# Kernel tuning notes

Measured on AMD Instinct MI355X. Metric: run time of the kernel, lower is better.

## Reference

```python
import jax, jax.numpy as jnp
import numpy as np

EPS = 1e-6
B, T, E, H = 2, 512, 1024, 256
NUM_BLOCK = 12


def normalize(x):
    # RMS-style normalization over the feature dim (no learned affine)
    return x * jax.lax.rsqrt(jnp.mean(x * x, axis=-1, keepdims=True) + EPS)


def bar_quadratic_causal(a, b):
    # y_i = (1/i) * sum_{j<=i} relu(a_i + b_j)   (causal prefix mean of pairwise relation)
    # a, b: [B, T, H]
    Tn = a.shape[1]
    pair = jax.nn.relu(a[:, :, None, :] + b[:, None, :, :])  # [B, T(i), T(j), H]
    mask = jnp.tril(jnp.ones((Tn, Tn), dtype=a.dtype))        # causal j<=i
    s = jnp.einsum('bijh,ij->bih', pair, mask)
    counts = jnp.arange(1, Tn + 1, dtype=a.dtype)[None, :, None]
    return s / counts


def setup_inputs() -> dict:
    key = jax.random.key(0)
    k0, k1, k2, k3 = jax.random.split(key, 4)
    x = jax.random.normal(k0, (B, T, E), dtype=jnp.float32)
    w1 = jax.random.normal(k1, (E, H), dtype=jnp.float32) * 0.02
    b1 = jnp.zeros((H,), dtype=jnp.float32)
    w2 = jax.random.normal(k2, (E, H), dtype=jnp.float32) * 0.02
    b2 = jnp.zeros((H,), dtype=jnp.float32)
    w3 = jax.random.normal(k3, (H, E), dtype=jnp.float32) * (0.02 / np.sqrt(NUM_BLOCK))
    b3 = jnp.zeros((E,), dtype=jnp.float32)
    return {"x": x, "w1": w1, "b1": b1, "w2": w2, "b2": b2, "w3": w3, "b3": b3}


def reference(x, w1, b1, w2, b2, w3, b3):
    r = normalize(x)
    a = r @ w1 + b1
    b = r @ w2 + b2
    # PreNorm == 'approx': normalize a and b separately
    a = normalize(a)
    b = normalize(b)
    r = bar_quadratic_causal(a, b)
    # PostNorm == 'yes'
    r = normalize(r)
    r = r @ w3 + b3
    return x + r
```

## Files before the change

kernel.cpp:

```cpp
#include <hip/hip_runtime.h>

#define EPSF 1e-6f
#define Bsz 2
#define Tn  512
#define En  1024
#define Hn  256
#define Mtot (Bsz * Tn)
typedef unsigned short us_t;
typedef unsigned int   u32_t;

typedef __attribute__((ext_vector_type(8))) short bf16x8;
typedef __attribute__((ext_vector_type(4))) float f32x4;
#define MFMA16(a, b, c) __builtin_amdgcn_mfma_f32_16x16x32_bf16((a), (b), (c), 0, 0, 0)

__device__ __forceinline__ us_t f2bf(float f) {
  union { float f; u32_t u; } x; x.f = f;
  u32_t r = (x.u + 0x7fffu + ((x.u >> 16) & 1u)) >> 16;
  return (us_t)r;
}
__device__ __forceinline__ float bf2f(us_t u) {
  union { u32_t u; float f; } x; x.u = ((u32_t)u) << 16; return x.f;
}
__device__ __forceinline__ uint2 pack4bf(float a, float b, float c, float d) {
  uint2 r;
  r.x = (u32_t)f2bf(a) | ((u32_t)f2bf(b) << 16);
  r.y = (u32_t)f2bf(c) | ((u32_t)f2bf(d) << 16);
  return r;
}
__device__ __forceinline__ float block_reduce_sum_256(float v, float* smem) {
  #pragma unroll
  for (int off = 32; off > 0; off >>= 1) v += __shfl_down(v, off, 64);
  const int wave = threadIdx.x >> 6;
  if ((threadIdx.x & 63) == 0) smem[wave] = v;
  __syncthreads();
  float s = smem[0] + smem[1] + smem[2] + smem[3];
  __syncthreads();
  return s;
}

__global__ __launch_bounds__(256) void k_prep(
    const float* __restrict__ x,
    const float* __restrict__ w1, const float* __restrict__ w2,
    const float* __restrict__ w3,
    us_t* __restrict__ xb, float* __restrict__ rs,
    us_t* __restrict__ w1t, us_t* __restrict__ w2t, us_t* __restrict__ w3t)
{
  const int b = blockIdx.x, t = threadIdx.x;

  if (b < 256) {
    const int wid = t >> 6, lane = t & 63;
    const int row = b * 4 + wid;
    const float4* xp = (const float4*)(x + (size_t)row * En);
    float4 v[4];
    #pragma unroll
    for (int i = 0; i < 4; ++i) v[i] = xp[lane + 64 * i];
    float ss = 0.f;
    #pragma unroll
    for (int i = 0; i < 4; ++i)
      ss += v[i].x*v[i].x + v[i].y*v[i].y + v[i].z*v[i].z + v[i].w*v[i].w;
    #pragma unroll
    for (int off = 32; off > 0; off >>= 1) ss += __shfl_xor(ss, off, 64);
    if (lane == 0) rs[row] = rsqrtf(ss * (1.0f / En) + EPSF);
    uint2* xo = (uint2*)(xb + (size_t)row * En);
    #pragma unroll
    for (int i = 0; i < 4; ++i)
      xo[lane + 64 * i] = pack4bf(v[i].x, v[i].y, v[i].z, v[i].w);
    return;
  }

  __shared__ float ts[32][33];
  const int i = b - 256;
  const float* src; us_t* dst; int R, C, tr, tc;
  if (i < 256)      { src = w1; dst = w1t; R = 1024; C = 256;  tr = i >> 3;  tc = i & 7; }
  else if (i < 512) { int k = i - 256; src = w2; dst = w2t; R = 1024; C = 256; tr = k >> 3; tc = k & 7; }
  else              { int k = i - 512; src = w3; dst = w3t; R = 256; C = 1024; tr = k >> 5; tc = k & 31; }

  const int r = t >> 3, c4 = (t & 7) * 4;
  float4 v = *(const float4*)(src + (size_t)(tr * 32 + r) * C + tc * 32 + c4);
  ts[r][c4 + 0] = v.x; ts[r][c4 + 1] = v.y; ts[r][c4 + 2] = v.z; ts[r][c4 + 3] = v.w;
  __syncthreads();
  float o0 = ts[c4 + 0][r], o1 = ts[c4 + 1][r], o2 = ts[c4 + 2][r], o3 = ts[c4 + 3][r];
  *(uint2*)(dst + (size_t)(tc * 32 + r) * R + tr * 32 + c4) = pack4bf(o0, o1, o2, o3);
}

__global__ __launch_bounds__(256, 4) void k_gemm(
    const us_t* __restrict__ xb,
    const us_t* __restrict__ w1t, const us_t* __restrict__ w2t,
    float* __restrict__ Praw)
{
  const int blk = blockIdx.x;
  const int mt = blk >> 4, nt = blk & 15;
  const int m0 = mt * 16, n0 = nt * 32;
  const int wid = threadIdx.x >> 6, lane = threadIdx.x & 63;
  const int lg = lane >> 4, lr = lane & 15;
  const int k0 = wid * 256;

  const us_t* ap = xb + (size_t)(m0 + lr) * En + k0 + lg * 8;
  const us_t* bbase = (n0 < Hn) ? (w1t + (size_t)n0 * En)
                                : (w2t + (size_t)(n0 - Hn) * En);
  const us_t* bp0 = bbase + (size_t)lr * En + k0 + lg * 8;
  const us_t* bp1 = bp0 + (size_t)16 * En;

  f32x4 acc0 = {0.f,0.f,0.f,0.f}, acc1 = acc0;

  #pragma unroll
  for (int s = 0; s < 8; ++s) {
    bf16x8 a  = *(const bf16x8*)(ap  + s * 32);
    bf16x8 b0 = *(const bf16x8*)(bp0 + s * 32);
    bf16x8 b1 = *(const bf16x8*)(bp1 + s * 32);
    acc0 = MFMA16(a, b0, acc0);
    acc1 = MFMA16(a, b1, acc1);
  }

  __shared__ float cmb[4][16][32];
  #pragma unroll
  for (int i = 0; i < 4; ++i) {
    cmb[wid][lg * 4 + i][lr]      = acc0[i];
    cmb[wid][lg * 4 + i][16 + lr] = acc1[i];
  }
  __syncthreads();

  #pragma unroll
  for (int e = 0; e < 2; ++e) {
    const int idx = threadIdx.x + e * 256;
    const int row = idx >> 5, col = idx & 31;
    float s = cmb[0][row][col] + cmb[1][row][col]
            + cmb[2][row][col] + cmb[3][row][col];
    Praw[(size_t)(m0 + row) * 512 + n0 + col] = s;
  }
}

__global__ __launch_bounds__(256) void k_norm(
    const float* __restrict__ Praw, const float* __restrict__ rs,
    const float* __restrict__ b1, const float* __restrict__ b2,
    us_t* __restrict__ A, us_t* __restrict__ BmT)
{
  const int rw = blockIdx.x * 4 + (threadIdx.x >> 6);
  const int lane = threadIdx.x & 63;
  const int which = rw >> 10, r = rw & 1023;
  const int h0 = lane * 4;

  float4 d = *(const float4*)(Praw + (size_t)r * 512 + which * Hn + h0);
  const float s0 = rs[r];
  const float* bias = which ? b2 : b1;
  float4 bv = *(const float4*)(bias + h0);
  float vx = d.x * s0 + bv.x, vy = d.y * s0 + bv.y;
  float vz = d.z * s0 + bv.z, vw = d.w * s0 + bv.w;

  float ss = vx*vx + vy*vy + vz*vz + vw*vw;
  #pragma unroll
  for (int o2 = 32; o2 > 0; o2 >>= 1) ss += __shfl_xor(ss, o2, 64);
  const float sc = rsqrtf(ss * (1.0f / Hn) + EPSF);

  if (!which) {
    *(uint2*)(A + (size_t)r * Hn + h0) = pack4bf(vx*sc, vy*sc, vz*sc, vw*sc);
  } else {
    const int bb = r >> 9, tcol = r & 511;
    us_t* bt = BmT + (size_t)bb * Hn * Tn + tcol;
    bt[(size_t)(h0 + 0) * Tn] = f2bf(vx * sc);
    bt[(size_t)(h0 + 1) * Tn] = f2bf(vy * sc);
    bt[(size_t)(h0 + 2) * Tn] = f2bf(vz * sc);
    bt[(size_t)(h0 + 3) * Tn] = f2bf(vw * sc);
  }
}

#define JCHB 32
__global__ __launch_bounds__(256) void k_bar(
    const us_t* __restrict__ A, const us_t* __restrict__ BmT,
    us_t* __restrict__ Yb)
{
  const int raw = blockIdx.x;
  const int sel = (raw < 256) ? raw : (511 - raw);
  const int bb  = raw >> 8;
  const int i0  = sel * 2;
  const int h   = threadIdx.x;
  const size_t baseA = (size_t)bb * Tn * Hn;
  const us_t* __restrict__ bt = BmT + (size_t)bb * Hn * Tn + (size_t)h * Tn;

  float av0 = bf2f(A[baseA + (size_t)i0 * Hn + h]);
  float av1 = bf2f(A[baseA + (size_t)(i0 + 1) * Hn + h]);
  float sum0 = 0.f, sum1 = 0.f;

  const int nfull = i0 & ~(JCHB - 1);
  bf16x8 c0[4], c1[4];

  #define LOADC(dst, jj) { _Pragma("unroll") \
    for (int q = 0; q < 4; ++q) dst[q] = *(const bf16x8*)(bt + (jj) + q * 8); }
  #define PROCF(srcb) { _Pragma("unroll") \
    for (int q = 0; q < 4; ++q) { _Pragma("unroll") \
      for (int e = 0; e < 8; ++e) { \
        float bv = bf2f((us_t)srcb[q][e]); \
        sum0 += fmaxf(av0 + bv, 0.f); \
        sum1 += fmaxf(av1 + bv, 0.f); } } }

  if (nfull > 0) {
    LOADC(c0, 0);
    int j = 0;
    while (true) {
      const bool m1 = (j + JCHB     < nfull);
      const bool m2 = (j + 2 * JCHB < nfull);
      if (m1) LOADC(c1, j + JCHB);
      PROCF(c0);
      j += JCHB;
      if (!m1) break;
      if (m2) LOADC(c0, j + JCHB);
      PROCF(c1);
      j += JCHB;
      if (!m2) break;
    }
  }
  {
    bf16x8 ct[4];
    LOADC(ct, nfull);
    const int lim = i0 - nfull;
    #pragma unroll
    for (int q = 0; q < 4; ++q)
      #pragma unroll
      for (int e = 0; e < 8; ++e) {
        const int jl = q * 8 + e;
        float bv = bf2f((us_t)ct[q][e]);
        sum0 += (jl <= lim)     ? fmaxf(av0 + bv, 0.f) : 0.f;
        sum1 += (jl <= lim + 1) ? fmaxf(av1 + bv, 0.f) : 0.f;
      }
  }
  #undef LOADC
  #undef PROCF

  __shared__ float red[4];
  {
    float ss = block_reduce_sum_256(sum0 * sum0, red);
    float c  = (float)(i0 + 1);
    float sc = rsqrtf(ss * (1.0f / Hn) + EPSF * c * c);
    Yb[baseA + (size_t)i0 * Hn + h] = f2bf(sum0 * sc);
  }
  {
    float ss = block_reduce_sum_256(sum1 * sum1, red);
    float c  = (float)(i0 + 2);
    float sc = rsqrtf(ss * (1.0f / Hn) + EPSF * c * c);
    Yb[baseA + (size_t)(i0 + 1) * Hn + h] = f2bf(sum1 * sc);
  }
}

__global__ __launch_bounds__(256, 4) void k_out(
    const us_t* __restrict__ Yb, const us_t* __restrict__ w3t,
    const float* __restrict__ x, const float* __restrict__ b3,
    float* __restrict__ out)
{
  const int wid = threadIdx.x >> 6, lane = threadIdx.x & 63;
  const int wg = blockIdx.x * 4 + wid;
  const int nt = wg & 31, mt = wg >> 5;
  const int m0 = mt * 16, n0 = nt * 32;
  const int lg = lane >> 4, lr = lane & 15;

  const us_t* ap  = Yb  + (size_t)(m0 + lr) * Hn + lg * 8;
  const us_t* bp0 = w3t + (size_t)(n0 + lr) * Hn + lg * 8;
  const us_t* bp1 = bp0 + (size_t)16 * Hn;

  f32x4 acc0 = {0.f,0.f,0.f,0.f}, acc1 = acc0;

  #pragma unroll
  for (int s = 0; s < 8; ++s) {
    bf16x8 a  = *(const bf16x8*)(ap  + s * 32);
    bf16x8 b0 = *(const bf16x8*)(bp0 + s * 32);
    bf16x8 b1 = *(const bf16x8*)(bp1 + s * 32);
    acc0 = MFMA16(a, b0, acc0);
    acc1 = MFMA16(a, b1, acc1);
  }

  const int row = m0 + lg * 4;
  const int c0 = n0 + lr, c1 = n0 + 16 + lr;
  const float bv0 = b3[c0], bv1 = b3[c1];
  #pragma unroll
  for (int i = 0; i < 4; ++i) {
    const size_t o0 = (size_t)(row + i) * En + c0;
    const size_t o1 = (size_t)(row + i) * En + c1;
    out[o0] = x[o0] + acc0[i] + bv0;
    out[o1] = x[o1] + acc1[i] + bv1;
  }
}

extern "C" void kernel_launch(void* const* d_in, const int* in_sizes, int n_in,
                              void* d_out, int out_size, void* d_ws, size_t ws_size,
                              hipStream_t stream) {
  const float* x  = (const float*)d_in[0];
  const float* w1 = (const float*)d_in[1];
  const float* b1 = (const float*)d_in[2];
  const float* w2 = (const float*)d_in[3];
  const float* b2 = (const float*)d_in[4];
  const float* w3 = (const float*)d_in[5];
  const float* b3 = (const float*)d_in[6];
  float* out = (float*)d_out;

  char* q = (char*)d_ws;
  float* Praw = (float*)q;  q += (size_t)Mtot * 512 * 4;
  us_t* xb    = (us_t*)q;   q += (size_t)Mtot * En * 2;
  us_t* w1t   = (us_t*)q;   q += (size_t)Hn * En * 2;
  us_t* w2t   = (us_t*)q;   q += (size_t)Hn * En * 2;
  us_t* w3t   = (us_t*)q;   q += (size_t)En * Hn * 2;
  us_t* A     = (us_t*)q;   q += (size_t)Mtot * Hn * 2;
  us_t* BmT   = (us_t*)q;   q += (size_t)Mtot * Hn * 2;
  us_t* Yb    = (us_t*)q;   q += (size_t)Mtot * Hn * 2;
  float* rs   = (float*)q;  q += (size_t)Mtot * 4;

  k_prep<<<1024, 256, 0, stream>>>(x, w1, w2, w3, xb, rs, w1t, w2t, w3t);
  k_gemm<<<1024, 256, 0, stream>>>(xb, w1t, w2t, Praw);
  k_norm<<<512,  256, 0, stream>>>(Praw, rs, b1, b2, A, BmT);
  k_bar <<<512,  256, 0, stream>>>(A, BmT, Yb);
  k_out <<<512,  256, 0, stream>>>(Yb, w3t, x, b3, out);
}
```

Before: 47.64 us.

## Switch to fp16 storage with packed-half bar loop, coalesced BmT transpose, finer k_out tiles

Stores intermediates in fp16 instead of bf16 and uses fp16 MFMA. The quadratic bar loop now does relu-add in packed half2 arithmetic, accumulating four pairs in fp16 before widening to fp32, which roughly halves the ALU work of the dominant kernel. k_norm writes the transposed B matrix through shared memory with 8-byte stores instead of strided 2-byte scatters. k_out uses 16x16 tiles per wave and twice as many blocks for more parallelism. The partial fp16 accumulation and the fp16 range of x could cost accuracy.

```diff
diff --git a/kernel.cpp b/kernel.cpp
--- a/kernel.cpp
+++ b/kernel.cpp
@@ -9,22 +9,23 @@
 typedef unsigned short us_t;
 typedef unsigned int   u32_t;
 
-typedef __attribute__((ext_vector_type(8))) short bf16x8;
-typedef __attribute__((ext_vector_type(4))) float f32x4;
-#define MFMA16(a, b, c) __builtin_amdgcn_mfma_f32_16x16x32_bf16((a), (b), (c), 0, 0, 0)
-
-__device__ __forceinline__ us_t f2bf(float f) {
-  union { float f; u32_t u; } x; x.f = f;
-  u32_t r = (x.u + 0x7fffu + ((x.u >> 16) & 1u)) >> 16;
-  return (us_t)r;
-}
-__device__ __forceinline__ float bf2f(us_t u) {
-  union { u32_t u; float f; } x; x.u = ((u32_t)u) << 16; return x.f;
-}
-__device__ __forceinline__ uint2 pack4bf(float a, float b, float c, float d) {
+typedef __attribute__((ext_vector_type(8))) __fp16 f16x8;
+typedef __attribute__((ext_vector_type(2))) __fp16 h2_t;
+typedef __attribute__((ext_vector_type(8))) short  short8;
+typedef __attribute__((ext_vector_type(4))) float  f32x4;
+#define MFMA16(a, b, c) __builtin_amdgcn_mfma_f32_16x16x32_f16((a), (b), (c), 0, 0, 0)
+
+__device__ __forceinline__ us_t f2h(float f) {
+  __fp16 h = (__fp16)f;
+  return __builtin_bit_cast(us_t, h);
+}
+__device__ __forceinline__ float h2f(us_t u) {
+  return (float)__builtin_bit_cast(__fp16, u);
+}
+__device__ __forceinline__ uint2 pack4h(float a, float b, float c, float d) {
   uint2 r;
-  r.x = (u32_t)f2bf(a) | ((u32_t)f2bf(b) << 16);
-  r.y = (u32_t)f2bf(c) | ((u32_t)f2bf(d) << 16);
+  r.x = (u32_t)f2h(a) | ((u32_t)f2h(b) << 16);
+  r.y = (u32_t)f2h(c) | ((u32_t)f2h(d) << 16);
   return r;
 }
 __device__ __forceinline__ float block_reduce_sum_256(float v, float* smem) {
@@ -64,7 +65,7 @@
     uint2* xo = (uint2*)(xb + (size_t)row * En);
     #pragma unroll
     for (int i = 0; i < 4; ++i)
-      xo[lane + 64 * i] = pack4bf(v[i].x, v[i].y, v[i].z, v[i].w);
+      xo[lane + 64 * i] = pack4h(v[i].x, v[i].y, v[i].z, v[i].w);
     return;
   }
 
@@ -80,7 +81,7 @@
   ts[r][c4 + 0] = v.x; ts[r][c4 + 1] = v.y; ts[r][c4 + 2] = v.z; ts[r][c4 + 3] = v.w;
   __syncthreads();
   float o0 = ts[c4 + 0][r], o1 = ts[c4 + 1][r], o2 = ts[c4 + 2][r], o3 = ts[c4 + 3][r];
-  *(uint2*)(dst + (size_t)(tc * 32 + r) * R + tr * 32 + c4) = pack4bf(o0, o1, o2, o3);
+  *(uint2*)(dst + (size_t)(tc * 32 + r) * R + tr * 32 + c4) = pack4h(o0, o1, o2, o3);
 }
 
 __global__ __launch_bounds__(256, 4) void k_gemm(
@@ -105,9 +106,9 @@
 
   #pragma unroll
   for (int s = 0; s < 8; ++s) {
-    bf16x8 a  = *(const bf16x8*)(ap  + s * 32);
-    bf16x8 b0 = *(const bf16x8*)(bp0 + s * 32);
-    bf16x8 b1 = *(const bf16x8*)(bp1 + s * 32);
+    f16x8 a  = *(const f16x8*)(ap  + s * 32);
+    f16x8 b0 = *(const f16x8*)(bp0 + s * 32);
+    f16x8 b1 = *(const f16x8*)(bp1 + s * 32);
     acc0 = MFMA16(a, b0, acc0);
     acc1 = MFMA16(a, b1, acc1);
   }
@@ -135,15 +136,33 @@
     const float* __restrict__ b1, const float* __restrict__ b2,
     us_t* __restrict__ A, us_t* __restrict__ BmT)
 {
-  const int rw = blockIdx.x * 4 + (threadIdx.x >> 6);
-  const int lane = threadIdx.x & 63;
-  const int which = rw >> 10, r = rw & 1023;
+  const int blk = blockIdx.x, t = threadIdx.x;
+  const int wid = t >> 6, lane = t & 63;
   const int h0 = lane * 4;
 
-  float4 d = *(const float4*)(Praw + (size_t)r * 512 + which * Hn + h0);
+  if (blk < 256) {
+    const int r = blk * 4 + wid;
+    float4 d = *(const float4*)(Praw + (size_t)r * 512 + h0);
+    const float s0 = rs[r];
+    float4 bv = *(const float4*)(b1 + h0);
+    float vx = d.x * s0 + bv.x, vy = d.y * s0 + bv.y;
+    float vz = d.z * s0 + bv.z, vw = d.w * s0 + bv.w;
+
+    float ss = vx*vx + vy*vy + vz*vz + vw*vw;
+    #pragma unroll
+    for (int o2 = 32; o2 > 0; o2 >>= 1) ss += __shfl_xor(ss, o2, 64);
+    const float sc = rsqrtf(ss * (1.0f / Hn) + EPSF);
+    *(uint2*)(A + (size_t)r * Hn + h0) = pack4h(vx*sc, vy*sc, vz*sc, vw*sc);
+    return;
+  }
+
+  __shared__ us_t ls[4][256];
+  const int r0 = (blk - 256) * 4;
+  const int r  = r0 + wid;
+
+  float4 d = *(const float4*)(Praw + (size_t)r * 512 + Hn + h0);
   const float s0 = rs[r];
-  const float* bias = which ? b2 : b1;
-  float4 bv = *(const float4*)(bias + h0);
+  float4 bv = *(const float4*)(b2 + h0);
   float vx = d.x * s0 + bv.x, vy = d.y * s0 + bv.y;
   float vz = d.z * s0 + bv.z, vw = d.w * s0 + bv.w;
 
@@ -152,16 +171,15 @@
   for (int o2 = 32; o2 > 0; o2 >>= 1) ss += __shfl_xor(ss, o2, 64);
   const float sc = rsqrtf(ss * (1.0f / Hn) + EPSF);
 
-  if (!which) {
-    *(uint2*)(A + (size_t)r * Hn + h0) = pack4bf(vx*sc, vy*sc, vz*sc, vw*sc);
-  } else {
-    const int bb = r >> 9, tcol = r & 511;
-    us_t* bt = BmT + (size_t)bb * Hn * Tn + tcol;
-    bt[(size_t)(h0 + 0) * Tn] = f2bf(vx * sc);
-    bt[(size_t)(h0 + 1) * Tn] = f2bf(vy * sc);
-    bt[(size_t)(h0 + 2) * Tn] = f2bf(vz * sc);
-    bt[(size_t)(h0 + 3) * Tn] = f2bf(vw * sc);
-  }
+  *(uint2*)&ls[wid][h0] = pack4h(vx*sc, vy*sc, vz*sc, vw*sc);
+  __syncthreads();
+
+  const int h = t;
+  u32_t w0  = (u32_t)ls[0][h] | ((u32_t)ls[1][h] << 16);
+  u32_t w1v = (u32_t)ls[2][h] | ((u32_t)ls[3][h] << 16);
+  const int bb   = r0 >> 9;
+  const int tcol = r0 & 511;
+  *(uint2*)(BmT + (size_t)bb * Hn * Tn + (size_t)h * Tn + tcol) = make_uint2(w0, w1v);
 }
 
 #define JCHB 32
@@ -177,21 +195,32 @@
   const size_t baseA = (size_t)bb * Tn * Hn;
   const us_t* __restrict__ bt = BmT + (size_t)bb * Hn * Tn + (size_t)h * Tn;
 
-  float av0 = bf2f(A[baseA + (size_t)i0 * Hn + h]);
-  float av1 = bf2f(A[baseA + (size_t)(i0 + 1) * Hn + h]);
+  const __fp16 a0h = __builtin_bit_cast(__fp16, A[baseA + (size_t)i0 * Hn + h]);
+  const __fp16 a1h = __builtin_bit_cast(__fp16, A[baseA + (size_t)(i0 + 1) * Hn + h]);
+  const float av0 = (float)a0h;
+  const float av1 = (float)a1h;
+  h2_t z2;  z2[0]  = (__fp16)0.f; z2[1]  = (__fp16)0.f;
+  h2_t a02; a02[0] = a0h;         a02[1] = a0h;
+  h2_t a12; a12[0] = a1h;         a12[1] = a1h;
   float sum0 = 0.f, sum1 = 0.f;
 
   const int nfull = i0 & ~(JCHB - 1);
-  bf16x8 c0[4], c1[4];
+  short8 c0[4], c1[4];
 
   #define LOADC(dst, jj) { _Pragma("unroll") \
-    for (int q = 0; q < 4; ++q) dst[q] = *(const bf16x8*)(bt + (jj) + q * 8); }
-  #define PROCF(srcb) { _Pragma("unroll") \
-    for (int q = 0; q < 4; ++q) { _Pragma("unroll") \
-      for (int e = 0; e < 8; ++e) { \
-        float bv = bf2f((us_t)srcb[q][e]); \
-        sum0 += fmaxf(av0 + bv, 0.f); \
-        sum1 += fmaxf(av1 + bv, 0.f); } } }
+    for (int q = 0; q < 4; ++q) dst[q] = *(const short8*)(bt + (jj) + q * 8); }
+  #define PROCP(buf) { _Pragma("unroll") \
+    for (int q = 0; q < 4; ++q) { \
+      const h2_t* ph = (const h2_t*)&buf[q]; \
+      h2_t p0 = z2, p1 = z2; \
+      _Pragma("unroll") \
+      for (int w2i = 0; w2i < 4; ++w2i) { \
+        h2_t bv2 = ph[w2i]; \
+        p0 += __builtin_elementwise_max(a02 + bv2, z2); \
+        p1 += __builtin_elementwise_max(a12 + bv2, z2); \
+      } \
+      sum0 += (float)p0[0] + (float)p0[1]; \
+      sum1 += (float)p1[0] + (float)p1[1]; } }
 
   if (nfull > 0) {
     LOADC(c0, 0);
@@ -200,17 +229,17 @@
       const bool m1 = (j + JCHB     < nfull);
       const bool m2 = (j + 2 * JCHB < nfull);
       if (m1) LOADC(c1, j + JCHB);
-      PROCF(c0);
+      PROCP(c0);
       j += JCHB;
       if (!m1) break;
       if (m2) LOADC(c0, j + JCHB);
-      PROCF(c1);
+      PROCP(c1);
       j += JCHB;
       if (!m2) break;
     }
   }
   {
-    bf16x8 ct[4];
+    short8 ct[4];
     LOADC(ct, nfull);
     const int lim = i0 - nfull;
     #pragma unroll
@@ -218,26 +247,26 @@
       #pragma unroll
       for (int e = 0; e < 8; ++e) {
         const int jl = q * 8 + e;
-        float bv = bf2f((us_t)ct[q][e]);
+        float bv = h2f((us_t)ct[q][e]);
         sum0 += (jl <= lim)     ? fmaxf(av0 + bv, 0.f) : 0.f;
         sum1 += (jl <= lim + 1) ? fmaxf(av1 + bv, 0.f) : 0.f;
       }
   }
   #undef LOADC
-  #undef PROCF
+  #undef PROCP
 
   __shared__ float red[4];
   {
     float ss = block_reduce_sum_256(sum0 * sum0, red);
     float c  = (float)(i0 + 1);
     float sc = rsqrtf(ss * (1.0f / Hn) + EPSF * c * c);
-    Yb[baseA + (size_t)i0 * Hn + h] = f2bf(sum0 * sc);
+    Yb[baseA + (size_t)i0 * Hn + h] = f2h(sum0 * sc);
   }
   {
     float ss = block_reduce_sum_256(sum1 * sum1, red);
     float c  = (float)(i0 + 2);
     float sc = rsqrtf(ss * (1.0f / Hn) + EPSF * c * c);
-    Yb[baseA + (size_t)(i0 + 1) * Hn + h] = f2bf(sum1 * sc);
+    Yb[baseA + (size_t)(i0 + 1) * Hn + h] = f2h(sum1 * sc);
   }
 }
 
@@ -248,34 +277,29 @@
 {
   const int wid = threadIdx.x >> 6, lane = threadIdx.x & 63;
   const int wg = blockIdx.x * 4 + wid;
-  const int nt = wg & 31, mt = wg >> 5;
-  const int m0 = mt * 16, n0 = nt * 32;
+  const int nt = wg & 63, mt = wg >> 6;
+  const int m0 = mt * 16, n0 = nt * 16;
   const int lg = lane >> 4, lr = lane & 15;
 
-  const us_t* ap  = Yb  + (size_t)(m0 + lr) * Hn + lg * 8;
-  const us_t* bp0 = w3t + (size_t)(n0 + lr) * Hn + lg * 8;
-  const us_t* bp1 = bp0 + (size_t)16 * Hn;
-
-  f32x4 acc0 = {0.f,0.f,0.f,0.f}, acc1 = acc0;
+  const us_t* ap = Yb  + (size_t)(m0 + lr) * Hn + lg * 8;
+  const us_t* bp = w3t + (size_t)(n0 + lr) * Hn + lg * 8;
+
+  f32x4 acc = {0.f,0.f,0.f,0.f};
 
   #pragma unroll
   for (int s = 0; s < 8; ++s) {
-    bf16x8 a  = *(const bf16x8*)(ap  + s * 32);
-    bf16x8 b0 = *(const bf16x8*)(bp0 + s * 32);
-    bf16x8 b1 = *(const bf16x8*)(bp1 + s * 32);
-    acc0 = MFMA16(a, b0, acc0);
-    acc1 = MFMA16(a, b1, acc1);
+    f16x8 a = *(const f16x8*)(ap + s * 32);
+    f16x8 b = *(const f16x8*)(bp + s * 32);
+    acc = MFMA16(a, b, acc);
   }
 
   const int row = m0 + lg * 4;
-  const int c0 = n0 + lr, c1 = n0 + 16 + lr;
-  const float bv0 = b3[c0], bv1 = b3[c1];
+  const int c = n0 + lr;
+  const float bv = b3[c];
   #pragma unroll
   for (int i = 0; i < 4; ++i) {
-    const size_t o0 = (size_t)(row + i) * En + c0;
-    const size_t o1 = (size_t)(row + i) * En + c1;
-    out[o0] = x[o0] + acc0[i] + bv0;
-    out[o1] = x[o1] + acc1[i] + bv1;
+    const size_t o = (size_t)(row + i) * En + c;
+    out[o] = x[o] + acc[i] + bv;
   }
 }
 
@@ -306,5 +330,5 @@
   k_gemm<<<1024, 256, 0, stream>>>(xb, w1t, w2t, Praw);
   k_norm<<<512,  256, 0, stream>>>(Praw, rs, b1, b2, A, BmT);
   k_bar <<<512,  256, 0, stream>>>(A, BmT, Yb);
-  k_out <<<512,  256, 0, stream>>>(Yb, w3t, x, b3, out);
-}
+  k_out <<<1024, 256, 0, stream>>>(Yb, w3t, x, b3, out);
+}
```

After: 47.48 us. About the same (-0.3%).
